# Performance work log

Hardware: AMD Instinct MI355X
Metric: run time of the kernel (lower is better)

The kernel has to match this reference:

```python
import jax, jax.numpy as jnp
import numpy as np
from jax import lax

B = 16
DEPTH = 24
D_MODEL = 192
D_INNER = 384   # expand=2
D_STATE = 16
D_CONV = 4
DT_RANK = 12    # ceil(192/16)
PATCH = 16
EPS = 1e-5


def setup_inputs() -> dict:
    key = jax.random.key(0)
    ks = jax.random.split(key, 24)
    def n(k, shape, s):
        return jax.random.normal(k, shape, jnp.float32) * s
    inp = {}
    inp["x_img"] = jax.random.normal(ks[0], (B, 3, 256, 256), jnp.float32)
    inp["z_img"] = jax.random.normal(ks[1], (B, 3, 128, 128), jnp.float32)
    # patch embed conv
    inp["patch_w"] = n(ks[2], (D_MODEL, 3, PATCH, PATCH), 0.02)
    inp["patch_b"] = jnp.zeros((D_MODEL,), jnp.float32)
    # abs pos embeds (token counts fixed by module: 256 for x, 64 for z)
    inp["pos_x"] = n(ks[3], (1, 256, D_MODEL), 0.02)
    inp["pos_z"] = n(ks[4], (1, 64, D_MODEL), 0.02)
    # per-layer norms (LayerNorm, rms_norm=False)
    inp["ln_w"] = jnp.ones((DEPTH, D_MODEL), jnp.float32)
    inp["ln_b"] = jnp.zeros((DEPTH, D_MODEL), jnp.float32)
    # Mamba mixer params (stacked over depth)
    inp["in_w"] = n(ks[5], (DEPTH, 2 * D_INNER, D_MODEL), 0.05)          # in_proj (no bias)
    inp["conv_w"] = n(ks[6], (DEPTH, D_INNER, D_CONV), 0.2)              # depthwise conv1d
    inp["conv_b"] = jnp.zeros((DEPTH, D_INNER), jnp.float32)
    inp["xproj_w"] = n(ks[7], (DEPTH, DT_RANK + 2 * D_STATE, D_INNER), 0.05)  # x_proj (no bias)
    inp["dt_w"] = n(ks[8], (DEPTH, D_INNER, DT_RANK), 0.1)               # dt_proj weight
    # dt bias ~ inverse-softplus of dt in [1e-3, 0.1] (Mamba init)
    dt = jnp.exp(jax.random.uniform(ks[9], (DEPTH, D_INNER)) * (np.log(0.1) - np.log(1e-3)) + np.log(1e-3))
    inp["dt_b"] = dt + jnp.log(-jnp.expm1(-dt))
    # A_log init: log(1..d_state) per channel
    inp["A_log"] = jnp.log(jnp.tile(jnp.arange(1, D_STATE + 1, dtype=jnp.float32), (DEPTH, D_INNER, 1)))
    inp["D_skip"] = jnp.ones((DEPTH, D_INNER), jnp.float32)
    inp["out_w"] = n(ks[10], (DEPTH, D_MODEL, D_INNER), 0.05)            # out_proj (no bias)
    inp["fnorm_w"] = jnp.ones((D_MODEL,), jnp.float32)
    inp["fnorm_b"] = jnp.zeros((D_MODEL,), jnp.float32)
    return inp


def _layer_norm(x, w, b):
    mu = jnp.mean(x, axis=-1, keepdims=True)
    var = jnp.mean(jnp.square(x - mu), axis=-1, keepdims=True)
    return (x - mu) * lax.rsqrt(var + EPS) * w + b


def _patch_embed(img, w, b):
    # Conv2d stride=patch, then flatten HW -> tokens
    y = lax.conv_general_dilated(img, w, (PATCH, PATCH), 'VALID',
                                 dimension_numbers=('NCHW', 'OIHW', 'NCHW'))
    y = y + b[None, :, None, None]
    Bn, D, H, W = y.shape
    return y.reshape(Bn, D, H * W).transpose(0, 2, 1)  # (B, HW, D)


def _ssm_scan(dA, dBu):
    # h_t = dA_t * h_{t-1} + dBu_t, parallel over time via associative scan
    def comb(e1, e2):
        a1, b1 = e1
        a2, b2 = e2
        return a2 * a1, a2 * b1 + b2
    _, h = lax.associative_scan(comb, (dA, dBu), axis=1)
    return h  # (B, L, D_INNER, D_STATE)


def _mamba(h, in_w, conv_w, conv_b, xproj_w, dt_w, dt_b, A_log, D_skip, out_w):
    # h: (B, L, D_MODEL)
    xz = h @ in_w.T                                   # (B, L, 2*D_INNER)
    xc, zg = jnp.split(xz, 2, axis=-1)
    # causal depthwise conv over time
    xt = xc.transpose(0, 2, 1)                        # (B, D_INNER, L)
    xt = lax.conv_general_dilated(xt, conv_w[:, None, :], (1,), [(D_CONV - 1, 0)],
                                  feature_group_count=D_INNER,
                                  dimension_numbers=('NCH', 'OIH', 'NCH'))
    xt = xt + conv_b[None, :, None]
    xc = jax.nn.silu(xt).transpose(0, 2, 1)           # (B, L, D_INNER)
    dbl = xc @ xproj_w.T                              # (B, L, dt_rank + 2*d_state)
    dt, Bm, Cm = jnp.split(dbl, [DT_RANK, DT_RANK + D_STATE], axis=-1)
    dt = jax.nn.softplus(dt @ dt_w.T + dt_b)          # (B, L, D_INNER)
    A = -jnp.exp(A_log)                               # (D_INNER, D_STATE)
    dA = jnp.exp(dt[..., None] * A)                   # (B, L, D_INNER, D_STATE)
    dBu = dt[..., None] * Bm[:, :, None, :] * xc[..., None]
    hs = _ssm_scan(dA, dBu)
    y = jnp.einsum('bldn,bln->bld', hs, Cm) + xc * D_skip
    y = y * jax.nn.silu(zg)
    return y @ out_w.T                                # (B, L, D_MODEL)


def reference(x_img, z_img, patch_w, patch_b, pos_x, pos_z, ln_w, ln_b,
              in_w, conv_w, conv_b, xproj_w, dt_w, dt_b, A_log, D_skip,
              out_w, fnorm_w, fnorm_b):
    x_tok = _patch_embed(x_img, patch_w, patch_b) + pos_x   # (B, 256, D)
    z_tok = _patch_embed(z_img, patch_w, patch_b) + pos_z   # (B, 64, D)
    hidden = jnp.concatenate([z_tok, x_tok], axis=1)        # (B, 320, D)
    residual = None
    for i in range(DEPTH):
        # fused add-norm prenorm: residual = hidden + residual; hidden = LN(residual)
        residual = hidden if residual is None else hidden + residual
        h_n = _layer_norm(residual, ln_w[i], ln_b[i])
        hidden = _mamba(h_n, in_w[i], conv_w[i], conv_b[i], xproj_w[i],
                        dt_w[i], dt_b[i], A_log[i], D_skip[i], out_w[i])
    residual = residual + hidden
    return _layer_norm(residual, fnorm_w, fnorm_b)          # (B, 320, D), final_pool_type='none'
```

## Files before the change

### kernel.cpp

```cpp
#include <hip/hip_runtime.h>
#include <hip/hip_bf16.h>

#define BB 16
#define DEPTH 24
#define DM 192
#define DI 384
#define DS 16
#define DC 4
#define DTR 12
#define LL 320
#define NX 256
#define NZ 64
#define NT (BB * LL)
#define NC 10
#define LC 32
#define EPSV 1e-5f

__device__ inline float siluf(float x) { return x / (1.f + __expf(-x)); }
__device__ inline float softplusf(float x) {
    return (x > 20.f) ? x : log1pf(expf(x));
}
__device__ inline float wave_sum64(float v) {
    #pragma unroll
    for (int o = 32; o > 0; o >>= 1) v += __shfl_xor(v, o);
    return v;
}

__global__ __launch_bounds__(256) void addnorm_kernel(const float* hidden,
                                                      float* __restrict__ residual,
                                                      float* hn,
                                                      const float* __restrict__ w,
                                                      const float* __restrict__ bias,
                                                      size_t off, int first) {
    int t = blockIdx.x * 4 + (threadIdx.x >> 6);
    int lane = threadIdx.x & 63;
    size_t base = (size_t)t * DM;
    float a = hidden[base + lane];
    float b = hidden[base + 64 + lane];
    float c = hidden[base + 128 + lane];
    if (!first) {
        a += residual[base + lane];
        b += residual[base + 64 + lane];
        c += residual[base + 128 + lane];
    }
    residual[base + lane] = a;
    residual[base + 64 + lane] = b;
    residual[base + 128 + lane] = c;
    float mu = wave_sum64(a + b + c) * (1.f / 192.f);
    float va = a - mu, vb = b - mu, vc = c - mu;
    float var = wave_sum64(va * va + vb * vb + vc * vc) * (1.f / 192.f);
    float inv = rsqrtf(var + EPSV);
    hn[base + lane]       = va * inv * w[off + lane]       + bias[off + lane];
    hn[base + 64 + lane]  = vb * inv * w[off + 64 + lane]  + bias[off + 64 + lane];
    hn[base + 128 + lane] = vc * inv * w[off + 128 + lane] + bias[off + 128 + lane];
}

template<int K, int KT, int NO>
__global__ __launch_bounds__(256) void gemm_rt(const float* __restrict__ x,
                                               const float* __restrict__ w,
                                               size_t woff,
                                               float* __restrict__ out, int N) {
    constexpr int NCOL = 64 * NO;
    constexpr int KC = KT / 4;
    __shared__ float xs[32][KT + 4];
    __shared__ float ws[NCOL][KT + 4];
    int t0 = blockIdx.x * 32;
    int j0 = blockIdx.y * NCOL;
    int lane = threadIdx.x & 63;
    int wv = threadIdx.x >> 6;
    float acc[8][NO];
    #pragma unroll
    for (int t = 0; t < 8; t++)
        #pragma unroll
        for (int o = 0; o < NO; o++) acc[t][o] = 0.f;

    for (int kt = 0; kt < K; kt += KT) {
        for (int idx = threadIdx.x; idx < 32 * KC; idx += 256) {
            int tt = idx / KC, kc = idx % KC;
            float4 v = *(const float4*)&x[(size_t)(t0 + tt) * K + kt + kc * 4];
            *(float4*)&xs[tt][kc * 4] = v;
        }
        for (int idx = threadIdx.x; idx < NCOL * KC; idx += 256) {
            int jj = idx / KC, kc = idx % KC;
            float4 v = *(const float4*)&w[woff + (size_t)(j0 + jj) * K + kt + kc * 4];
            *(float4*)&ws[jj][kc * 4] = v;
        }
        __syncthreads();
        #pragma unroll 2
        for (int kk = 0; kk < KT; kk += 4) {
            float4 xv[8];
            #pragma unroll
            for (int t = 0; t < 8; t++)
                xv[t] = *(const float4*)&xs[wv * 8 + t][kk];
            #pragma unroll
            for (int o = 0; o < NO; o++) {
                float4 wv4 = *(const float4*)&ws[lane + 64 * o][kk];
                #pragma unroll
                for (int t = 0; t < 8; t++)
                    acc[t][o] += xv[t].x * wv4.x + xv[t].y * wv4.y
                               + xv[t].z * wv4.z + xv[t].w * wv4.w;
            }
        }
        __syncthreads();
    }
    #pragma unroll
    for (int t = 0; t < 8; t++)
        #pragma unroll
        for (int o = 0; o < NO; o++)
            out[(size_t)(t0 + wv * 8 + t) * N + j0 + lane + 64 * o] = acc[t][o];
}

__global__ __launch_bounds__(256) void patch_rt(const float* __restrict__ x_img,
                                                const float* __restrict__ z_img,
                                                const float* __restrict__ w,
                                                const float* __restrict__ bias,
                                                const float* __restrict__ pos_x,
                                                const float* __restrict__ pos_z,
                                                float* __restrict__ hidden) {
    __shared__ float xs[32][100];
    __shared__ float ws[64][100];
    bool isx = blockIdx.x < (BB * NX / 32);
    const float* img = isx ? x_img : z_img;
    const float* pos = isx ? pos_x : pos_z;
    int side = isx ? 16 : 8;
    int tok_off = isx ? NZ : 0;
    int ntok = side * side;
    int pt0 = (isx ? blockIdx.x : blockIdx.x - BB * NX / 32) * 32;
    int j0 = blockIdx.y * 64;
    int S = side * 16;
    int lane = threadIdx.x & 63;
    int wv = threadIdx.x >> 6;
    float acc[8];
    #pragma unroll
    for (int t = 0; t < 8; t++) acc[t] = 0.f;

    for (int kt = 0; kt < 768; kt += 96) {
        for (int idx = threadIdx.x; idx < 32 * 24; idx += 256) {
            int tt = idx / 24, kc = idx % 24;
            int k = kt + kc * 4;
            int c = k >> 8, p = k & 255, pi = p >> 4, pj = p & 15;
            int patch = pt0 + tt;
            int b = patch / ntok, t = patch % ntok;
            int ph = t / side, pw = t % side;
            float4 v = *(const float4*)&img[((size_t)(b * 3 + c) * S + ph * 16 + pi) * S
                                            + pw * 16 + pj];
            *(float4*)&xs[tt][kc * 4] = v;
        }
        for (int idx = threadIdx.x; idx < 64 * 24; idx += 256) {
            int jj = idx / 24, kc = idx % 24;
            float4 v = *(const float4*)&w[(size_t)(j0 + jj) * 768 + kt + kc * 4];
            *(float4*)&ws[jj][kc * 4] = v;
        }
        __syncthreads();
        #pragma unroll 2
        for (int kk = 0; kk < 96; kk += 4) {
            float4 xv[8];
            #pragma unroll
            for (int t = 0; t < 8; t++)
                xv[t] = *(const float4*)&xs[wv * 8 + t][kk];
            float4 wv4 = *(const float4*)&ws[lane][kk];
            #pragma unroll
            for (int t = 0; t < 8; t++)
                acc[t] += xv[t].x * wv4.x + xv[t].y * wv4.y
                        + xv[t].z * wv4.z + xv[t].w * wv4.w;
        }
        __syncthreads();
    }
    float bj = bias[j0 + lane];
    #pragma unroll
    for (int t = 0; t < 8; t++) {
        int patch = pt0 + wv * 8 + t;
        int b = patch / ntok, tk = patch % ntok;
        hidden[((size_t)b * LL + tok_off + tk) * DM + j0 + lane] =
            acc[t] + bj + pos[(size_t)tk * DM + j0 + lane];
    }
}

__global__ __launch_bounds__(256) void xpd_kernel(const float* __restrict__ xz,
                                                  const float* __restrict__ cw,
                                                  const float* __restrict__ cb,
                                                  const float* __restrict__ xpw,
                                                  const float* __restrict__ dtw,
                                                  const float* __restrict__ dtbias,
                                                  float* __restrict__ xc,
                                                  float* __restrict__ dbl,
                                                  float* __restrict__ dtbuf,
                                                  int layer) {
    __shared__ float smem[5760];
    float* xs   = smem;
    float* ws   = smem + 832;
    float* sdbl = smem;
    float* sdtw = smem + 768;

    int t0 = blockIdx.x * 16;
    int l0 = t0 % LL;
    int lane = threadIdx.x & 63;
    int wv = threadIdx.x >> 6;
    const float* cwl = cw  + (size_t)layer * DI * DC;
    const float* cbl = cb  + (size_t)layer * DI;
    const float* xpl = xpw + (size_t)layer * 44 * DI;
    float acc[4] = {0.f, 0.f, 0.f, 0.f};

    for (int kt = 0; kt < DI; kt += 48) {
        for (int idx = threadIdx.x; idx < 16 * 12; idx += 256) {
            int tt = idx / 12, kc = idx % 12;
            int d = kt + kc * 4;
            float4 a = *(const float4*)&cbl[d];
            float4 cw0 = *(const float4*)&cwl[(size_t)(d + 0) * 4];
            float4 cw1 = *(const float4*)&cwl[(size_t)(d + 1) * 4];
            float4 cw2 = *(const float4*)&cwl[(size_t)(d + 2) * 4];
            float4 cw3 = *(const float4*)&cwl[(size_t)(d + 3) * 4];
            const float* c0 = &cw0.x;
            const float* c1 = &cw1.x;
            const float* c2 = &cw2.x;
            const float* c3 = &cw3.x;
            #pragma unroll
            for (int rr = 0; rr < 4; rr++) {
                int l = l0 + tt - 3 + rr;
                float4 v = make_float4(0.f, 0.f, 0.f, 0.f);
                if (l >= 0)
                    v = *(const float4*)&xz[(size_t)(t0 + tt - 3 + rr) * 768 + d];
                a.x += c0[rr] * v.x;
                a.y += c1[rr] * v.y;
                a.z += c2[rr] * v.z;
                a.w += c3[rr] * v.w;
            }
            a.x = siluf(a.x); a.y = siluf(a.y); a.z = siluf(a.z); a.w = siluf(a.w);
            *(float4*)&xs[tt * 52 + kc * 4] = a;
            *(float4*)&xc[(size_t)(t0 + tt) * DI + d] = a;
        }
        for (int idx = threadIdx.x; idx < 64 * 12; idx += 256) {
            int jj = idx / 12, kc = idx % 12;
            float4 v = make_float4(0.f, 0.f, 0.f, 0.f);
            if (jj < 44)
                v = *(const float4*)&xpl[(size_t)jj * DI + kt + kc * 4];
            *(float4*)&ws[jj * 52 + kc * 4] = v;
        }
        __syncthreads();
        const float* wr0 = ws + lane * 52;
        #pragma unroll 4
        for (int kk = 0; kk < 48; kk += 4) {
            float4 xv0 = *(const float4*)&xs[(wv * 4 + 0) * 52 + kk];
            float4 xv1 = *(const float4*)&xs[(wv * 4 + 1) * 52 + kk];
            float4 xv2 = *(const float4*)&xs[(wv * 4 + 2) * 52 + kk];
            float4 xv3 = *(const float4*)&xs[(wv * 4 + 3) * 52 + kk];
            float4 wv4 = *(const float4*)&wr0[kk];
            acc[0] += xv0.x * wv4.x + xv0.y * wv4.y + xv0.z * wv4.z + xv0.w * wv4.w;
            acc[1] += xv1.x * wv4.x + xv1.y * wv4.y + xv1.z * wv4.z + xv1.w * wv4.w;
            acc[2] += xv2.x * wv4.x + xv2.y * wv4.y + xv2.z * wv4.z + xv2.w * wv4.w;
            acc[3] += xv3.x * wv4.x + xv3.y * wv4.y + xv3.z * wv4.z + xv3.w * wv4.w;
        }
        __syncthreads();
    }
    if (lane < 44) {
        #pragma unroll
        for (int t = 0; t < 4; t++) {
            sdbl[(wv * 4 + t) * 48 + lane] = acc[t];
            dbl[(size_t)(t0 + wv * 4 + t) * 44 + lane] = acc[t];
        }
    }
    const float* dwl = dtw + (size_t)layer * DI * DTR;
    for (int idx = threadIdx.x; idx < DI * DTR; idx += 256) {
        int d = idx / 12, rr = idx % 12;
        sdtw[d * 13 + rr] = dwl[idx];
    }
    __syncthreads();
    const float* dbb = dtbias + (size_t)layer * DI;
    for (int idx = threadIdx.x; idx < 16 * DI; idx += 256) {
        int tt = idx / DI, d = idx % DI;
        float a = dbb[d];
        const float* br = sdbl + tt * 48;
        const float* wr = sdtw + d * 13;
        #pragma unroll
        for (int rr = 0; rr < 12; rr++) a += br[rr] * wr[rr];
        dtbuf[(size_t)(t0 + tt) * DI + d] = softplusf(a);
    }
}

__global__ __launch_bounds__(256) void scanA(const float* __restrict__ dt,
                                             const float* __restrict__ xc,
                                             const float* __restrict__ dbl,
                                             const float* __restrict__ A_log,
                                             float* __restrict__ Pout,
                                             float* __restrict__ Hout,
                                             size_t aoff) {
    int Q = blockIdx.x * 64 + (threadIdx.x >> 2);
    int n0 = threadIdx.x & 3;
    int d = Q % DI;
    int bc = Q / DI;
    int b = bc / NC, c = bc % NC;
    float4 Al = *(const float4*)&A_log[aoff + (size_t)d * DS + n0 * 4];
    float A0 = -expf(Al.x), A1 = -expf(Al.y), A2 = -expf(Al.z), A3 = -expf(Al.w);
    float h0 = 0.f, h1 = 0.f, h2 = 0.f, h3 = 0.f;
    float P0 = 1.f, P1 = 1.f, P2 = 1.f, P3 = 1.f;
    int tbase = b * LL + c * LC;
    for (int l = 0; l < LC; l++) {
        size_t t = (size_t)tbase + l;
        float dtv = dt[t * DI + d];
        float xcv = xc[t * DI + d];
        float4 B4 = *(const float4*)&dbl[t * 44 + DTR + n0 * 4];
        float s = dtv * xcv;
        float e0 = __expf(dtv * A0), e1 = __expf(dtv * A1);
        float e2 = __expf(dtv * A2), e3 = __expf(dtv * A3);
        h0 = e0 * h0 + s * B4.x;  P0 *= e0;
        h1 = e1 * h1 + s * B4.y;  P1 *= e1;
        h2 = e2 * h2 + s * B4.z;  P2 *= e2;
        h3 = e3 * h3 + s * B4.w;  P3 *= e3;
    }
    size_t gi = (size_t)Q * 16 + n0 * 4;
    *(float4*)&Pout[gi] = make_float4(P0, P1, P2, P3);
    *(float4*)&Hout[gi] = make_float4(h0, h1, h2, h3);
}

__global__ __launch_bounds__(256) void scanC(const float* __restrict__ dt,
                                             const float* xc,
                                             const float* __restrict__ dbl,
                                             const float* __restrict__ xz,
                                             const float* __restrict__ A_log,
                                             const float* __restrict__ Dskip,
                                             const float* __restrict__ Pin,
                                             const float* __restrict__ Hin,
                                             float* y,
                                             size_t aoff, size_t doff) {
    int Q = blockIdx.x * 64 + (threadIdx.x >> 2);
    int n0 = threadIdx.x & 3;
    int d = Q % DI;
    int bc = Q / DI;
    int b = bc / NC, c = bc % NC;
    float h0 = 0.f, h1 = 0.f, h2 = 0.f, h3 = 0.f;
    for (int cc = 0; cc < c; cc++) {
        size_t gi = ((size_t)(b * NC + cc) * DI + d) * 16 + n0 * 4;
        float4 P4 = *(const float4*)&Pin[gi];
        float4 H4 = *(const float4*)&Hin[gi];
        h0 = P4.x * h0 + H4.x;
        h1 = P4.y * h1 + H4.y;
        h2 = P4.z * h2 + H4.z;
        h3 = P4.w * h3 + H4.w;
    }
    float4 Al = *(const float4*)&A_log[aoff + (size_t)d * DS + n0 * 4];
    float A0 = -expf(Al.x), A1 = -expf(Al.y), A2 = -expf(Al.z), A3 = -expf(Al.w);
    float Dv = Dskip[doff + d];
    int tbase = b * LL + c * LC;
    for (int l = 0; l < LC; l++) {
        size_t t = (size_t)tbase + l;
        float dtv = dt[t * DI + d];
        float xcv = xc[t * DI + d];
        float4 B4 = *(const float4*)&dbl[t * 44 + DTR + n0 * 4];
        float4 C4 = *(const float4*)&dbl[t * 44 + DTR + DS + n0 * 4];
        float s = dtv * xcv;
        float e0 = __expf(dtv * A0), e1 = __expf(dtv * A1);
        float e2 = __expf(dtv * A2), e3 = __expf(dtv * A3);
        h0 = e0 * h0 + s * B4.x;
        h1 = e1 * h1 + s * B4.y;
        h2 = e2 * h2 + s * B4.z;
        h3 = e3 * h3 + s * B4.w;
        float p = h0 * C4.x + h1 * C4.y + h2 * C4.z + h3 * C4.w;
        p += __shfl_xor(p, 1);
        p += __shfl_xor(p, 2);
        if (n0 == 0) {
            float zg = xz[t * (2 * DI) + DI + d];
            y[t * DI + d] = (p + xcv * Dv) * siluf(zg);
        }
    }
}

__global__ __launch_bounds__(256) void final_kernel(const float* __restrict__ hidden,
                                                    const float* __restrict__ residual,
                                                    const float* __restrict__ w,
                                                    const float* __restrict__ bias,
                                                    float* __restrict__ out) {
    int t = blockIdx.x * 4 + (threadIdx.x >> 6);
    int lane = threadIdx.x & 63;
    size_t base = (size_t)t * DM;
    float a = residual[base + lane]       + hidden[base + lane];
    float b = residual[base + 64 + lane]  + hidden[base + 64 + lane];
    float c = residual[base + 128 + lane] + hidden[base + 128 + lane];
    float mu = wave_sum64(a + b + c) * (1.f / 192.f);
    float va = a - mu, vb = b - mu, vc = c - mu;
    float var = wave_sum64(va * va + vb * vb + vc * vc) * (1.f / 192.f);
    float inv = rsqrtf(var + EPSV);
    out[base + lane]       = va * inv * w[lane]       + bias[lane];
    out[base + 64 + lane]  = vb * inv * w[64 + lane]  + bias[64 + lane];
    out[base + 128 + lane] = vc * inv * w[128 + lane] + bias[128 + lane];
}

extern "C" void kernel_launch(void* const* d_in, const int* in_sizes, int n_in,
                              void* d_out, int out_size, void* d_ws, size_t ws_size,
                              hipStream_t stream) {
    const float* x_img   = (const float*)d_in[0];
    const float* z_img   = (const float*)d_in[1];
    const float* patch_w = (const float*)d_in[2];
    const float* patch_b = (const float*)d_in[3];
    const float* pos_x   = (const float*)d_in[4];
    const float* pos_z   = (const float*)d_in[5];
    const float* ln_w    = (const float*)d_in[6];
    const float* ln_b    = (const float*)d_in[7];
    const float* in_w    = (const float*)d_in[8];
    const float* conv_w  = (const float*)d_in[9];
    const float* conv_b  = (const float*)d_in[10];
    const float* xproj_w = (const float*)d_in[11];
    const float* dt_w    = (const float*)d_in[12];
    const float* dt_b    = (const float*)d_in[13];
    const float* A_log   = (const float*)d_in[14];
    const float* D_skip  = (const float*)d_in[15];
    const float* out_w   = (const float*)d_in[16];
    const float* fnorm_w = (const float*)d_in[17];
    const float* fnorm_b = (const float*)d_in[18];

    float* hidden   = (float*)d_ws;
    float* residual = hidden   + (size_t)NT * DM;
    float* xz       = residual + (size_t)NT * DM;
    float* xc       = xz       + (size_t)NT * 2 * DI;
    float* dbl      = xc       + (size_t)NT * DI;
    float* dtbuf    = dbl      + (size_t)NT * 44;
    float* scanP    = dtbuf    + (size_t)NT * DI;
    float* scanH    = scanP    + (size_t)BB * NC * DI * 16;
    float* hn       = hidden;
    float* yb       = xc;

    {
        dim3 gp((BB * NX + BB * NZ) / 32, 3);
        patch_rt<<<gp, 256, 0, stream>>>(x_img, z_img, patch_w, patch_b,
                                         pos_x, pos_z, hidden);
    }

    const int scan_blocks = BB * NC * DI / 64;
    for (int i = 0; i < DEPTH; i++) {
        addnorm_kernel<<<NT / 4, 256, 0, stream>>>(
            hidden, residual, hn, ln_w, ln_b, (size_t)i * DM, i == 0 ? 1 : 0);
        {
            dim3 g(NT / 32, 3);
            gemm_rt<192, 24, 4><<<g, 256, 0, stream>>>(
                hn, in_w, (size_t)i * 768 * 192, xz, 768);
        }
        xpd_kernel<<<NT / 16, 256, 0, stream>>>(
            xz, conv_w, conv_b, xproj_w, dt_w, dt_b, xc, dbl, dtbuf, i);
        scanA<<<scan_blocks, 256, 0, stream>>>(
            dtbuf, xc, dbl, A_log, scanP, scanH, (size_t)i * DI * DS);
        scanC<<<scan_blocks, 256, 0, stream>>>(
            dtbuf, xc, dbl, xz, A_log, D_skip, scanP, scanH, yb,
            (size_t)i * DI * DS, (size_t)i * DI);
        {
            dim3 g(NT / 32, 3);
            gemm_rt<384, 96, 1><<<g, 256, 0, stream>>>(
                yb, out_w, (size_t)i * 192 * 384, hidden, 192);
        }
    }

    final_kernel<<<NT / 4, 256, 0, stream>>>(hidden, residual, fnorm_w, fnorm_b,
                                             (float*)d_out);
}
```

Before: 3.968 ms.

## Fuse two-pass chunked scan into one kernel with shared-memory chunk carry

Merges the chunk-summary scan pass and the output scan pass into a single kernel. Each block now covers all 10 chunks for 8 channels of one batch element and exchanges chunk decay products and states through shared memory instead of global buffers. This removes one launch per layer and the global P/H round trip. In exchange each block runs 320 threads over 768 blocks, which changes occupancy. The chunk-local recurrence is still recomputed in the second phase, so dt, xc and B are read twice as before.

```diff
diff --git a/kernel.cpp b/kernel.cpp
--- a/kernel.cpp
+++ b/kernel.cpp
@@ -277,23 +277,29 @@
     }
 }
 
-__global__ __launch_bounds__(256) void scanA(const float* __restrict__ dt,
-                                             const float* __restrict__ xc,
-                                             const float* __restrict__ dbl,
-                                             const float* __restrict__ A_log,
-                                             float* __restrict__ Pout,
-                                             float* __restrict__ Hout,
-                                             size_t aoff) {
-    int Q = blockIdx.x * 64 + (threadIdx.x >> 2);
+__global__ __launch_bounds__(320) void scan_fused(const float* __restrict__ dt,
+                                                  const float* xc,
+                                                  const float* __restrict__ dbl,
+                                                  const float* __restrict__ xz,
+                                                  const float* __restrict__ A_log,
+                                                  const float* __restrict__ Dskip,
+                                                  float* y,
+                                                  size_t aoff, size_t doff) {
+    __shared__ float sP[NC * 8 * 16];
+    __shared__ float sH[NC * 8 * 16];
+    int b = blockIdx.x / (DI / 8);
+    int dbase = (blockIdx.x % (DI / 8)) * 8;
+    int quad = threadIdx.x >> 2;
     int n0 = threadIdx.x & 3;
-    int d = Q % DI;
-    int bc = Q / DI;
-    int b = bc / NC, c = bc % NC;
+    int c = quad >> 3;
+    int dl = quad & 7;
+    int d = dbase + dl;
     float4 Al = *(const float4*)&A_log[aoff + (size_t)d * DS + n0 * 4];
     float A0 = -expf(Al.x), A1 = -expf(Al.y), A2 = -expf(Al.z), A3 = -expf(Al.w);
+    int tbase = b * LL + c * LC;
+
     float h0 = 0.f, h1 = 0.f, h2 = 0.f, h3 = 0.f;
     float P0 = 1.f, P1 = 1.f, P2 = 1.f, P3 = 1.f;
-    int tbase = b * LL + c * LC;
     for (int l = 0; l < LC; l++) {
         size_t t = (size_t)tbase + l;
         float dtv = dt[t * DI + d];
@@ -307,40 +313,23 @@
         h2 = e2 * h2 + s * B4.z;  P2 *= e2;
         h3 = e3 * h3 + s * B4.w;  P3 *= e3;
     }
-    size_t gi = (size_t)Q * 16 + n0 * 4;
-    *(float4*)&Pout[gi] = make_float4(P0, P1, P2, P3);
-    *(float4*)&Hout[gi] = make_float4(h0, h1, h2, h3);
-}
-
-__global__ __launch_bounds__(256) void scanC(const float* __restrict__ dt,
-                                             const float* xc,
-                                             const float* __restrict__ dbl,
-                                             const float* __restrict__ xz,
-                                             const float* __restrict__ A_log,
-                                             const float* __restrict__ Dskip,
-                                             const float* __restrict__ Pin,
-                                             const float* __restrict__ Hin,
-                                             float* y,
-                                             size_t aoff, size_t doff) {
-    int Q = blockIdx.x * 64 + (threadIdx.x >> 2);
-    int n0 = threadIdx.x & 3;
-    int d = Q % DI;
-    int bc = Q / DI;
-    int b = bc / NC, c = bc % NC;
-    float h0 = 0.f, h1 = 0.f, h2 = 0.f, h3 = 0.f;
+    int si = quad * 16 + n0 * 4;
+    *(float4*)&sP[si] = make_float4(P0, P1, P2, P3);
+    *(float4*)&sH[si] = make_float4(h0, h1, h2, h3);
+    __syncthreads();
+
+    h0 = h1 = h2 = h3 = 0.f;
     for (int cc = 0; cc < c; cc++) {
-        size_t gi = ((size_t)(b * NC + cc) * DI + d) * 16 + n0 * 4;
-        float4 P4 = *(const float4*)&Pin[gi];
-        float4 H4 = *(const float4*)&Hin[gi];
+        int gi = (cc * 8 + dl) * 16 + n0 * 4;
+        float4 P4 = *(const float4*)&sP[gi];
+        float4 H4 = *(const float4*)&sH[gi];
         h0 = P4.x * h0 + H4.x;
         h1 = P4.y * h1 + H4.y;
         h2 = P4.z * h2 + H4.z;
         h3 = P4.w * h3 + H4.w;
     }
-    float4 Al = *(const float4*)&A_log[aoff + (size_t)d * DS + n0 * 4];
-    float A0 = -expf(Al.x), A1 = -expf(Al.y), A2 = -expf(Al.z), A3 = -expf(Al.w);
+
     float Dv = Dskip[doff + d];
-    int tbase = b * LL + c * LC;
     for (int l = 0; l < LC; l++) {
         size_t t = (size_t)tbase + l;
         float dtv = dt[t * DI + d];
@@ -413,8 +402,6 @@
     float* xc       = xz       + (size_t)NT * 2 * DI;
     float* dbl      = xc       + (size_t)NT * DI;
     float* dtbuf    = dbl      + (size_t)NT * 44;
-    float* scanP    = dtbuf    + (size_t)NT * DI;
-    float* scanH    = scanP    + (size_t)BB * NC * DI * 16;
     float* hn       = hidden;
     float* yb       = xc;
 
@@ -424,7 +411,7 @@
                                          pos_x, pos_z, hidden);
     }
 
-    const int scan_blocks = BB * NC * DI / 64;
+    const int scan_blocks = BB * (DI / 8);
     for (int i = 0; i < DEPTH; i++) {
         addnorm_kernel<<<NT / 4, 256, 0, stream>>>(
             hidden, residual, hn, ln_w, ln_b, (size_t)i * DM, i == 0 ? 1 : 0);
@@ -435,10 +422,8 @@
         }
         xpd_kernel<<<NT / 16, 256, 0, stream>>>(
             xz, conv_w, conv_b, xproj_w, dt_w, dt_b, xc, dbl, dtbuf, i);
-        scanA<<<scan_blocks, 256, 0, stream>>>(
-            dtbuf, xc, dbl, A_log, scanP, scanH, (size_t)i * DI * DS);
-        scanC<<<scan_blocks, 256, 0, stream>>>(
-            dtbuf, xc, dbl, xz, A_log, D_skip, scanP, scanH, yb,
+        scan_fused<<<scan_blocks, 320, 0, stream>>>(
+            dtbuf, xc, dbl, xz, A_log, D_skip, yb,
             (size_t)i * DI * DS, (size_t)i * DI);
         {
             dim3 g(NT / 32, 3);
```

After: 3.946 ms. Within noise of the previous version (-0.5%).
